# Optimization experiments

Hardware: AMD Instinct MI355X
Metric: run time of the kernel (lower is better)

Reference implementation:

```python
import jax, jax.numpy as jnp
import numpy as np

N_NODES = 20000
N_EDGES = 160000
MUL0, MUL1 = 32, 16          # 32x0e + 16x1o for both in and out irreps
EDGE_FEAT = 128
HIDDEN = 128
W_SIZES = [MUL0*MUL0, MUL1*MUL0, MUL0*MUL1, MUL1*MUL1, MUL1*MUL1]  # uvw weights per path (sh muls are 1)
W_OFF = np.cumsum([0] + W_SIZES).tolist()
W_NUMEL = W_OFF[-1]          # 2560
EPS_LN = 1e-5

_e = np.zeros((3, 3, 3), np.float32)
for i, j, k in [(0, 1, 2), (1, 2, 0), (2, 0, 1)]:
    _e[i, j, k] = 1.0
    _e[i, k, j] = -1.0
EPS3 = jnp.asarray(_e)  # Levi-Civita for 1o x 1o -> 1o path


def setup_inputs() -> dict:
    key = jax.random.key(0)
    ks = jax.random.split(key, 8)
    node_attr = jax.random.normal(ks[0], (N_NODES, MUL0 + 3 * MUL1), jnp.float32)
    edge_index = jax.random.randint(ks[1], (2, N_EDGES), 0, N_NODES)
    edge_attr = jax.random.normal(ks[2], (N_EDGES, EDGE_FEAT), jnp.float32)
    edge_sh = jax.random.normal(ks[3], (N_EDGES, 4), jnp.float32)
    s1 = float(1.0 / np.sqrt(EDGE_FEAT))
    s2 = float(1.0 / np.sqrt(HIDDEN))
    fc_w1 = jax.random.uniform(ks[4], (EDGE_FEAT, HIDDEN), jnp.float32, -s1, s1)
    fc_b1 = jnp.zeros((HIDDEN,), jnp.float32)
    fc_w2 = jax.random.uniform(ks[5], (HIDDEN, W_NUMEL), jnp.float32, -s2, s2)
    fc_b2 = jnp.zeros((W_NUMEL,), jnp.float32)
    # LayerNorm params: mean_shift is ones for scalar (0e) irreps, zeros for 1o
    mean_shift = jnp.concatenate(
        [jnp.ones((1, MUL0, 1), jnp.float32), jnp.zeros((1, MUL1, 1), jnp.float32)], axis=1)
    affine_weight = jnp.ones((MUL0 + MUL1,), jnp.float32) + 0.1 * jax.random.normal(ks[6], (MUL0 + MUL1,), jnp.float32)
    affine_bias = 0.02 * jax.random.normal(ks[7], (MUL0,), jnp.float32)
    return dict(node_attr=node_attr, edge_attr=edge_attr, edge_sh=edge_sh,
                fc_w1=fc_w1, fc_b1=fc_b1, fc_w2=fc_w2, fc_b2=fc_b2,
                mean_shift=mean_shift, affine_weight=affine_weight,
                affine_bias=affine_bias, edge_index=edge_index)


def _forward(node_attr, edge_attr, edge_sh, fc_w1, fc_b1, fc_w2, fc_b2,
             mean_shift, affine_weight, affine_bias, edge_index):
    edge_src, edge_dst = edge_index[0], edge_index[1]
    # gather source-of-message node features per edge
    x = node_attr[edge_dst]                          # [E, 80]
    x0 = x[:, :MUL0]                                 # [E, 32]   l=0 scalars
    x1 = x[:, MUL0:].reshape(-1, MUL1, 3)            # [E, 16, 3] l=1 vectors
    sh0 = edge_sh[:, 0]                              # [E]
    sh1 = edge_sh[:, 1:4]                            # [E, 3]

    # per-edge TP weights from edge features (SimpleLinear: Lin-ReLU-Lin, dropout=0)
    w = jnp.maximum(edge_attr @ fc_w1 + fc_b1, 0.0) @ fc_w2 + fc_b2   # [E, 2560]
    w1 = w[:, W_OFF[0]:W_OFF[1]].reshape(-1, MUL0, MUL0)
    w2 = w[:, W_OFF[1]:W_OFF[2]].reshape(-1, MUL1, MUL0)
    w3 = w[:, W_OFF[2]:W_OFF[3]].reshape(-1, MUL0, MUL1)
    w4 = w[:, W_OFF[3]:W_OFF[4]].reshape(-1, MUL1, MUL1)
    w5 = w[:, W_OFF[4]:W_OFF[5]].reshape(-1, MUL1, MUL1)

    # e3nn FullyConnectedTensorProduct normalization (component + element):
    # coeff = sqrt(ir_out.dim / sum_of_fan_in_over_paths_to_that_output)
    c0 = float(np.sqrt(1.0 / (MUL0 + MUL1)))            # -> 0e: fan 32+16
    c1 = float(np.sqrt(3.0 / (MUL0 + MUL1 + MUL1)))     # -> 1o: fan 32+16+16
    is3 = float(1.0 / np.sqrt(3.0))  # wigner-3j (110),(011),(101)
    is6 = float(1.0 / np.sqrt(6.0))  # wigner-3j (111)

    out0 = c0 * (jnp.einsum('eu,e,euw->ew', x0, sh0, w1)
                 + is3 * jnp.einsum('eui,ei,euw->ew', x1, sh1, w2))            # [E, 32]
    out1 = c1 * (is3 * jnp.einsum('eu,ek,euw->ewk', x0, sh1, w3)
                 + is3 * jnp.einsum('eui,e,euw->ewi', x1, sh0, w4)
                 + is6 * jnp.einsum('ijk,eui,ej,euw->ewk', EPS3, x1, sh1, w5)) # [E, 16, 3]
    tp = jnp.concatenate([out0, out1.reshape(-1, MUL1 * 3)], axis=-1)          # [E, 80]

    # scatter-mean over destination (edge_src) nodes
    seg = jax.ops.segment_sum(tp, edge_src, num_segments=N_NODES)
    cnt = jax.ops.segment_sum(jnp.ones((tp.shape[0],), tp.dtype), edge_src, num_segments=N_NODES)
    out = seg / jnp.maximum(cnt, 1.0)[:, None]

    # residual (out irreps == in irreps, so F.pad is a no-op)
    out = out + node_attr

    # equivariant LayerNorm (normalization='component')
    f0 = out[:, :MUL0].reshape(-1, MUL0, 1)
    f0 = f0 - jnp.mean(f0, axis=1, keepdims=True) * mean_shift[:, :MUL0]
    n0 = jnp.mean(jnp.mean(f0 * f0, axis=-1), axis=1, keepdims=True)           # [N, 1]
    n0 = jax.lax.rsqrt(n0 + EPS_LN) * affine_weight[None, :MUL0]               # [N, 32]
    f0 = f0 * n0[:, :, None] + affine_bias[None, :, None]

    f1 = out[:, MUL0:].reshape(-1, MUL1, 3)
    f1 = f1 - jnp.mean(f1, axis=1, keepdims=True) * mean_shift[:, MUL0:]       # mean_shift=0 here
    n1 = jnp.mean(jnp.mean(f1 * f1, axis=-1), axis=1, keepdims=True)
    n1 = jax.lax.rsqrt(n1 + EPS_LN) * affine_weight[None, MUL0:]
    f1 = f1 * n1[:, :, None]

    return jnp.concatenate([f0.reshape(-1, MUL0), f1.reshape(-1, MUL1 * 3)], axis=-1)


def reference(node_attr, edge_attr, edge_sh, fc_w1, fc_b1, fc_w2, fc_b2,
              mean_shift, affine_weight, affine_bias, edge_index):
    return _forward(node_attr, edge_attr, edge_sh, fc_w1, fc_b1, fc_w2, fc_b2,
                    mean_shift, affine_weight, affine_bias, edge_index)
```

## Files before the change

### kernel.cpp

```cpp
#include <hip/hip_runtime.h>

typedef __attribute__((ext_vector_type(8))) short short8;
typedef __attribute__((ext_vector_type(4))) short bfx4;
typedef __attribute__((ext_vector_type(4))) float floatx4;

#define N_NODES 20000
#define N_EDGES 160000
#define TILE_E 128
#define EBLK (N_EDGES / TILE_E)

#define C0f   0.14433756729740643f
#define C1f   0.21650635094610965f
#define IS3   0.5773502691896258f
#define IS6   0.4082482904638631f
#define EPS_LN 1e-5f

#define W1F_OFF 0
#define W2F_OFF 32768
#define CNT_OFF 688128

__device__ __forceinline__ short f2bf(float f) {
    unsigned u = __float_as_uint(f);
    u += 0x7fff + ((u >> 16) & 1);
    return (short)(u >> 16);
}
__device__ __forceinline__ float bf2f(short s) {
    return __uint_as_float(((unsigned)(unsigned short)s) << 16);
}

__device__ __forceinline__ short8 load8_bf16(const float* p) {
    const float4* q = (const float4*)p;
    float4 f0 = q[0], f1 = q[1];
    short8 s;
    s[0]=f2bf(f0.x); s[1]=f2bf(f0.y); s[2]=f2bf(f0.z); s[3]=f2bf(f0.w);
    s[4]=f2bf(f1.x); s[5]=f2bf(f1.y); s[6]=f2bf(f1.z); s[7]=f2bf(f1.w);
    return s;
}

__device__ __forceinline__ floatx4 mfma4(const short8* a, short8 b0, short8 b1,
                                         short8 b2, short8 b3, float bias) {
    floatx4 C = {bias, bias, bias, bias};
    C = __builtin_amdgcn_mfma_f32_16x16x32_bf16(a[0], b0, C, 0, 0, 0);
    C = __builtin_amdgcn_mfma_f32_16x16x32_bf16(a[1], b1, C, 0, 0, 0);
    C = __builtin_amdgcn_mfma_f32_16x16x32_bf16(a[2], b2, C, 0, 0, 0);
    C = __builtin_amdgcn_mfma_f32_16x16x32_bf16(a[3], b3, C, 0, 0, 0);
    return C;
}

__device__ __forceinline__ int xsw(int row, int el) {
    return row * 64 + ((el & 3) | ((((el >> 2) ^ row) & 15) << 2));
}
__device__ __forceinline__ bfx4 ldx(const short* base, int row, int gran) {
    return *(const bfx4*)(base + row * 64 + (((gran ^ row) & 15) << 2));
}

__device__ __forceinline__ int hsw(int row, int col) {
    return row * 128 + (col & 7) + ((((col >> 3) ^ (row & 15)) & 15) << 3);
}

__global__ __launch_bounds__(256)
void prep_kernel(const float* __restrict__ fc_w1, const float* __restrict__ fc_w2,
                 short* __restrict__ w1f, short* __restrict__ w2f,
                 float* __restrict__ cnt, float* __restrict__ out) {
    int g = blockIdx.x * 256 + threadIdx.x;
    if (g < N_NODES) cnt[g] = 0.0f;
    float4 z = {0.f, 0.f, 0.f, 0.f};
    for (int i = g; i < 400000; i += 43008) ((float4*)out)[i] = z;
    if (g < 2048) {
        int ln = g & 15, qd = (g >> 4) & 3, kt = (g >> 6) & 3, t = g >> 8;
        int n = t * 16 + ln, kb = kt * 32 + qd * 8;
        short8 s;
        #pragma unroll
        for (int j = 0; j < 8; ++j) s[j] = f2bf(fc_w1[(kb + j) * 128 + n]);
        *(short8*)(w1f + g * 8) = s;
    } else {
        int g2 = g - 2048;
        if (g2 < 40960) {
            int ln = g2 & 15, qd = (g2 >> 4) & 3, kt = (g2 >> 6) & 3, t = g2 >> 8;
            int n = t * 16 + ln, kb = kt * 32 + qd * 8;
            short8 s;
            #pragma unroll
            for (int j = 0; j < 8; ++j) s[j] = f2bf(fc_w2[(kb + j) * 2560 + n]);
            int p = (t < 128) ? t : (t < 144 ? 128 + 2 * (t - 128) : 129 + 2 * (t - 144));
            *(short8*)(w2f + (size_t)p * 2048 + (g2 & 255) * 8) = s;
        }
    }
}

__global__ __launch_bounds__(256, 2)
void edge_kernel(const float* __restrict__ node_attr,
                 const float* __restrict__ edge_attr,
                 const float* __restrict__ edge_sh,
                 const float* __restrict__ fc_b1,
                 const float* __restrict__ fc_b2,
                 const int*   __restrict__ edge_index,
                 const short* __restrict__ w1f,
                 const short* __restrict__ w2f,
                 float* __restrict__ accum,
                 float* __restrict__ cnt)
{
    __shared__ __align__(16) short s_pool[128 * 128];
    __shared__ __align__(16) short s_w2[2 * 4096];
    __shared__ float s_sh[128 * 4];
    __shared__ int   s_src[128];
    __shared__ int   s_dst[128];

    short* s_H    = s_pool;
    short* s_x0t  = s_pool;
    short* s_x1t  = s_pool + 4096;
    short* s_x1dt = s_pool + 10240;

    const int tid  = threadIdx.x;
    const int e0   = blockIdx.x * TILE_E;
    const int lane = tid & 63;
    const int wv   = tid >> 6;

    float4 stA, stB;
    {
        const float4* sp = (const float4*)w2f;
        stA = sp[tid]; stB = sp[tid + 256];
    }

    if (tid < 128) {
        int s = edge_index[e0 + tid];
        int d = edge_index[N_EDGES + e0 + tid];
        s_src[tid] = s; s_dst[tid] = d;
        atomicAdd(&cnt[s], 1.0f);
    }
    s_sh[tid]       = edge_sh[(size_t)e0 * 4 + tid];
    s_sh[tid + 256] = edge_sh[(size_t)e0 * 4 + tid + 256];
    __syncthreads();

    const int ln   = lane & 15;
    const int qd   = lane >> 4;
    const int eb0  = wv * 32 + qd * 4;
    const int eb1  = eb0 + 16;
    const int half = wv >> 1;
    const int gr0  = (wv & 1) * 8 + qd;
    const int gr1  = gr0 + 4;
    const short* x0b  = s_x0t  + half * 2048;
    const short* x1b  = s_x1t  + half * 3072;
    const short* x1db = s_x1dt + half * 1024;

    {
        short8 a1[2][4];
        #pragma unroll
        for (int g = 0; g < 2; ++g) {
            const float* ap = edge_attr + (size_t)(e0 + wv*32 + g*16 + ln) * 128 + qd * 8;
            #pragma unroll
            for (int kt = 0; kt < 4; ++kt) a1[g][kt] = load8_bf16(ap + kt * 32);
        }
        #pragma unroll
        for (int t = 0; t < 8; ++t) {
            const short* bp = w1f + t * 2048 + lane * 8;
            short8 b0 = *(const short8*)bp;
            short8 b1 = *(const short8*)(bp + 512);
            short8 b2 = *(const short8*)(bp + 1024);
            short8 b3 = *(const short8*)(bp + 1536);
            float bias = fc_b1[t * 16 + ln];
            #pragma unroll
            for (int g = 0; g < 2; ++g) {
                floatx4 C = mfma4(a1[g], b0, b1, b2, b3, bias);
                #pragma unroll
                for (int r = 0; r < 4; ++r)
                    s_H[hsw(wv*32 + g*16 + qd*4 + r, t*16 + ln)] = f2bf(fmaxf(C[r], 0.f));
            }
        }
    }

    short8 a2[2][4];
    #pragma unroll
    for (int g = 0; g < 2; ++g) {
        const int row = wv*32 + g*16 + ln;
        #pragma unroll
        for (int kt = 0; kt < 4; ++kt)
            a2[g][kt] = *(const short8*)(s_H + row * 128 +
                                         (((qd + 4*kt) ^ (row & 15)) << 3));
    }
    __syncthreads();

    #pragma unroll
    for (int i = 0; i < 40; ++i) {
        int f = tid + i * 256;
        int e = f / 80, c = f % 80;
        float v = node_attr[(size_t)s_dst[e] * 80 + c];
        int hf = e >> 6, el = e & 63;
        if (c < 32) s_x0t[hf * 2048 + xsw(c, el)] = f2bf(v);
        else        s_x1t[hf * 3072 + xsw(c - 32, el)] = f2bf(v);
    }
    #pragma unroll
    for (int i = 0; i < 8; ++i) {
        int it = tid + i * 256;
        int e = it >> 4, u = it & 15;
        const float* xp = node_attr + (size_t)s_dst[e] * 80 + 32 + u * 3;
        float d = xp[0] * s_sh[e*4+1] + xp[1] * s_sh[e*4+2] + xp[2] * s_sh[e*4+3];
        s_x1dt[(e >> 6) * 1024 + xsw(u, e & 63)] = f2bf(d);
    }
    {
        float4* dp = (float4*)s_w2;
        dp[tid] = stA; dp[tid + 256] = stB;
        const float4* sp = (const float4*)(w2f + 4096);
        stA = sp[tid]; stB = sp[tid + 256];
    }
    __syncthreads();

    auto stage_step = [&](int cg) {
        if (cg + 1 < 80) {
            float4* dp = (float4*)(s_w2 + ((cg + 1) & 1) * 4096);
            dp[tid] = stA; dp[tid + 256] = stB;
        }
        if (cg + 2 < 80) {
            const float4* sp = (const float4*)(w2f + (size_t)(cg + 2) * 4096);
            stA = sp[tid]; stB = sp[tid + 256];
        }
    };

    float r0lo[2][4] = {}, r0hi[2][4] = {}, r1lo[2][4] = {}, r1hi[2][4] = {};

    #pragma unroll 1
    for (int c = 0; c < 32; ++c) {
        stage_step(c);
        const short* bp = s_w2 + (c & 1) * 4096 + lane * 8;
        short8 L0 = *(const short8*)bp,          L1 = *(const short8*)(bp + 512);
        short8 L2 = *(const short8*)(bp + 1024), L3 = *(const short8*)(bp + 1536);
        short8 H0 = *(const short8*)(bp + 2048), H1 = *(const short8*)(bp + 2560);
        short8 H2 = *(const short8*)(bp + 3072), H3 = *(const short8*)(bp + 3584);
        float blo = fc_b2[c * 32 + ln], bhi = fc_b2[c * 32 + 16 + ln];
        #pragma unroll
        for (int g = 0; g < 2; ++g) {
            floatx4 Clo = mfma4(a2[g], L0, L1, L2, L3, blo);
            floatx4 Chi = mfma4(a2[g], H0, H1, H2, H3, bhi);
            bfx4 xs = ldx(x0b, c, g ? gr1 : gr0);
            #pragma unroll
            for (int r = 0; r < 4; ++r) {
                float a = bf2f(xs[r]);
                r0lo[g][r] += a * Clo[r];
                r0hi[g][r] += a * Chi[r];
            }
        }
        __syncthreads();
    }
    #pragma unroll 1
    for (int c2 = 0; c2 < 16; ++c2) {
        stage_step(32 + c2);
        const short* bp = s_w2 + ((32 + c2) & 1) * 4096 + lane * 8;
        short8 L0 = *(const short8*)bp,          L1 = *(const short8*)(bp + 512);
        short8 L2 = *(const short8*)(bp + 1024), L3 = *(const short8*)(bp + 1536);
        short8 H0 = *(const short8*)(bp + 2048), H1 = *(const short8*)(bp + 2560);
        short8 H2 = *(const short8*)(bp + 3072), H3 = *(const short8*)(bp + 3584);
        float blo = fc_b2[1024 + c2 * 32 + ln], bhi = fc_b2[1024 + c2 * 32 + 16 + ln];
        #pragma unroll
        for (int g = 0; g < 2; ++g) {
            floatx4 Clo = mfma4(a2[g], L0, L1, L2, L3, blo);
            floatx4 Chi = mfma4(a2[g], H0, H1, H2, H3, bhi);
            bfx4 xs = ldx(x1db, c2, g ? gr1 : gr0);
            #pragma unroll
            for (int r = 0; r < 4; ++r) {
                float a = bf2f(xs[r]);
                r1lo[g][r] += a * Clo[r];
                r1hi[g][r] += a * Chi[r];
            }
        }
        __syncthreads();
    }
    #pragma unroll
    for (int g = 0; g < 2; ++g)
        #pragma unroll
        for (int r = 0; r < 4; ++r) {
            int e = (g ? eb1 : eb0) + r;
            float sh0 = s_sh[e*4];
            int base = s_src[e] * 80;
            atomicAdd(&accum[base + ln],      C0f * (sh0 * r0lo[g][r] + IS3 * r1lo[g][r]));
            atomicAdd(&accum[base + 16 + ln], C0f * (sh0 * r0hi[g][r] + IS3 * r1hi[g][r]));
        }

    float r3[2][4] = {};
    float r4[2][4][3] = {};
    float r5[2][4][3] = {};

    #pragma unroll 1
    for (int c3 = 0; c3 < 16; ++c3) {
        stage_step(48 + c3);
        const short* bb = s_w2 + ((48 + c3) & 1) * 4096 + lane * 8;
        #pragma unroll
        for (int t = 0; t < 2; ++t) {
            const int u = 2 * c3 + t;
            const short* bp = bb + t * 2048;
            short8 b0 = *(const short8*)bp,          b1 = *(const short8*)(bp + 512);
            short8 b2 = *(const short8*)(bp + 1024), b3 = *(const short8*)(bp + 1536);
            float bias = fc_b2[1536 + u * 16 + ln];
            #pragma unroll
            for (int g = 0; g < 2; ++g) {
                floatx4 C = mfma4(a2[g], b0, b1, b2, b3, bias);
                bfx4 xs = ldx(x0b, u, g ? gr1 : gr0);
                #pragma unroll
                for (int r = 0; r < 4; ++r)
                    r3[g][r] += bf2f(xs[r]) * C[r];
            }
        }
        __syncthreads();
    }
    #pragma unroll 1
    for (int c4 = 0; c4 < 16; ++c4) {
        const int cg = 64 + c4;
        stage_step(cg);
        const short* bb = s_w2 + (cg & 1) * 4096 + lane * 8;
        short8 F0 = *(const short8*)bb,          F1 = *(const short8*)(bb + 512);
        short8 F2 = *(const short8*)(bb + 1024), F3 = *(const short8*)(bb + 1536);
        short8 G0 = *(const short8*)(bb + 2048), G1 = *(const short8*)(bb + 2560);
        short8 G2 = *(const short8*)(bb + 3072), G3 = *(const short8*)(bb + 3584);
        float b4 = fc_b2[2048 + c4 * 16 + ln], b5 = fc_b2[2304 + c4 * 16 + ln];
        #pragma unroll
        for (int g = 0; g < 2; ++g) {
            floatx4 C4 = mfma4(a2[g], F0, F1, F2, F3, b4);
            floatx4 C5 = mfma4(a2[g], G0, G1, G2, G3, b5);
            int gr = (g ? gr1 : gr0);
            bfx4 x0s = ldx(x1b, c4*3 + 0, gr);
            bfx4 x1s = ldx(x1b, c4*3 + 1, gr);
            bfx4 x2s = ldx(x1b, c4*3 + 2, gr);
            #pragma unroll
            for (int r = 0; r < 4; ++r) {
                float a0 = bf2f(x0s[r]), a1 = bf2f(x1s[r]), a2v = bf2f(x2s[r]);
                r4[g][r][0] += a0 * C4[r];  r5[g][r][0] += a0 * C5[r];
                r4[g][r][1] += a1 * C4[r];  r5[g][r][1] += a1 * C5[r];
                r4[g][r][2] += a2v * C4[r]; r5[g][r][2] += a2v * C5[r];
            }
        }
        if (c4 < 15) __syncthreads();
    }
    #pragma unroll
    for (int g = 0; g < 2; ++g)
        #pragma unroll
        for (int r = 0; r < 4; ++r) {
            int e = (g ? eb1 : eb0) + r;
            float sh0 = s_sh[e*4], sa = s_sh[e*4+1], sb = s_sh[e*4+2], sc = s_sh[e*4+3];
            int base = s_src[e] * 80;
            float t3 = C1f * IS3 * r3[g][r];
            float s0 = C1f * IS3 * sh0;
            float c6 = C1f * IS6;
            float v50 = r5[g][r][1] * sc - r5[g][r][2] * sb;
            float v51 = r5[g][r][2] * sa - r5[g][r][0] * sc;
            float v52 = r5[g][r][0] * sb - r5[g][r][1] * sa;
            atomicAdd(&accum[base + 32 + ln*3 + 0], sa * t3 + s0 * r4[g][r][0] + c6 * v50);
            atomicAdd(&accum[base + 32 + ln*3 + 1], sb * t3 + s0 * r4[g][r][1] + c6 * v51);
            atomicAdd(&accum[base + 32 + ln*3 + 2], sc * t3 + s0 * r4[g][r][2] + c6 * v52);
        }
}

__global__ __launch_bounds__(256)
void node_kernel(const float* __restrict__ node_attr,
                 const float* __restrict__ mean_shift,
                 const float* __restrict__ aw,
                 const float* __restrict__ ab,
                 const float* __restrict__ cnt,
                 float* __restrict__ out)
{
    __shared__ float sv[64 * 85];
    __shared__ float s_inv[64];
    const int tid = threadIdx.x;
    const int n0  = blockIdx.x * 64;

    if (tid < 64) {
        int n = n0 + tid;
        s_inv[tid] = (n < N_NODES) ? 1.0f / fmaxf(cnt[n], 1.0f) : 0.0f;
    }
    __syncthreads();

    #pragma unroll
    for (int i = 0; i < 20; ++i) {
        int idx = tid + i * 256;
        int r = idx / 80, cch = idx % 80;
        int n = n0 + r;
        if (n < N_NODES) {
            float o = out[(size_t)n * 80 + cch];
            float a = node_attr[(size_t)n * 80 + cch];
            sv[r * 85 + cch] = o * s_inv[r] + a;
        }
    }
    __syncthreads();

    if (tid < 64 && n0 + tid < N_NODES) {
        float v[80];
        const float* sp = sv + tid * 85;
        #pragma unroll
        for (int k = 0; k < 80; ++k) v[k] = sp[k];

        float m0 = 0.f;
        #pragma unroll
        for (int u = 0; u < 32; ++u) m0 += v[u];
        m0 *= (1.0f / 32.0f);
        float n0v = 0.f;
        #pragma unroll
        for (int u = 0; u < 32; ++u) {
            float f = v[u] - m0 * mean_shift[u];
            v[u] = f;
            n0v += f * f;
        }
        n0v = rsqrtf(n0v * (1.0f / 32.0f) + EPS_LN);
        #pragma unroll
        for (int u = 0; u < 32; ++u) v[u] = v[u] * (n0v * aw[u]) + ab[u];

        float m1[3] = {0.f, 0.f, 0.f};
        #pragma unroll
        for (int u = 0; u < 16; ++u)
            #pragma unroll
            for (int i = 0; i < 3; ++i) m1[i] += v[32 + u*3 + i];
        #pragma unroll
        for (int i = 0; i < 3; ++i) m1[i] *= (1.0f / 16.0f);
        float n1 = 0.f;
        #pragma unroll
        for (int u = 0; u < 16; ++u)
            #pragma unroll
            for (int i = 0; i < 3; ++i) {
                float f = v[32 + u*3 + i] - m1[i] * mean_shift[32 + u];
                v[32 + u*3 + i] = f;
                n1 += f * f;
            }
        n1 = rsqrtf(n1 * (1.0f / 48.0f) + EPS_LN);
        #pragma unroll
        for (int u = 0; u < 16; ++u)
            #pragma unroll
            for (int i = 0; i < 3; ++i)
                v[32 + u*3 + i] *= (n1 * aw[32 + u]);

        float* wp = sv + tid * 85;
        #pragma unroll
        for (int k = 0; k < 80; ++k) wp[k] = v[k];
    }
    __syncthreads();

    #pragma unroll
    for (int i = 0; i < 20; ++i) {
        int idx = tid + i * 256;
        int r = idx / 80, cch = idx % 80;
        int n = n0 + r;
        if (n < N_NODES) out[(size_t)n * 80 + cch] = sv[r * 85 + cch];
    }
}

extern "C" void kernel_launch(void* const* d_in, const int* in_sizes, int n_in,
                              void* d_out, int out_size, void* d_ws, size_t ws_size,
                              hipStream_t stream) {
    const float* node_attr  = (const float*)d_in[0];
    const float* edge_attr  = (const float*)d_in[1];
    const float* edge_sh    = (const float*)d_in[2];
    const float* fc_w1      = (const float*)d_in[3];
    const float* fc_b1      = (const float*)d_in[4];
    const float* fc_w2      = (const float*)d_in[5];
    const float* fc_b2      = (const float*)d_in[6];
    const float* mean_shift = (const float*)d_in[7];
    const float* aw         = (const float*)d_in[8];
    const float* ab         = (const float*)d_in[9];
    const int*   edge_index = (const int*)d_in[10];
    float* out = (float*)d_out;

    short* w1f = (short*)((char*)d_ws + W1F_OFF);
    short* w2f = (short*)((char*)d_ws + W2F_OFF);
    float* cnt = (float*)((char*)d_ws + CNT_OFF);

    prep_kernel<<<(2048 + 40960 + 255) / 256, 256, 0, stream>>>(fc_w1, fc_w2, w1f, w2f,
                                                                cnt, out);
    edge_kernel<<<EBLK, 256, 0, stream>>>(node_attr, edge_attr, edge_sh,
                                          fc_b1, fc_b2, edge_index,
                                          w1f, w2f, out, cnt);
    node_kernel<<<(N_NODES + 63) / 64, 256, 0, stream>>>(node_attr, mean_shift,
                                                         aw, ab, cnt, out);
}
```

Before: 363.3 us.

## Use two waves per edge tile, each handling 64 edges

The edge kernel now runs 128 threads (2 waves) per 128-edge tile instead of 4 waves, so each wave processes 64 edges (4 row groups) rather than 32. Each B fragment of the weight matrix loaded from LDS is reused across four MFMAs instead of two, which halves LDS reads of weights per edge. Per-thread staging of weights grows to four float4 registers. The cost is fewer waves per CU to hide latency and much higher register pressure, since the accumulator arrays double and could spill under launch_bounds(128,2).

```diff
diff --git a/kernel.cpp b/kernel.cpp
--- a/kernel.cpp
+++ b/kernel.cpp
@@ -87,7 +87,7 @@
     }
 }
 
-__global__ __launch_bounds__(256, 2)
+__global__ __launch_bounds__(128, 2)
 void edge_kernel(const float* __restrict__ node_attr,
                  const float* __restrict__ edge_attr,
                  const float* __restrict__ edge_sh,
@@ -115,38 +115,35 @@
     const int lane = tid & 63;
     const int wv   = tid >> 6;
 
-    float4 stA, stB;
+    float4 stA, stB, stC, stD;
     {
         const float4* sp = (const float4*)w2f;
-        stA = sp[tid]; stB = sp[tid + 256];
-    }
-
-    if (tid < 128) {
+        stA = sp[tid]; stB = sp[tid + 128]; stC = sp[tid + 256]; stD = sp[tid + 384];
+    }
+
+    {
         int s = edge_index[e0 + tid];
         int d = edge_index[N_EDGES + e0 + tid];
         s_src[tid] = s; s_dst[tid] = d;
         atomicAdd(&cnt[s], 1.0f);
     }
-    s_sh[tid]       = edge_sh[(size_t)e0 * 4 + tid];
-    s_sh[tid + 256] = edge_sh[(size_t)e0 * 4 + tid + 256];
+    #pragma unroll
+    for (int i = 0; i < 4; ++i)
+        s_sh[tid + i * 128] = edge_sh[(size_t)e0 * 4 + tid + i * 128];
     __syncthreads();
 
     const int ln   = lane & 15;
     const int qd   = lane >> 4;
-    const int eb0  = wv * 32 + qd * 4;
-    const int eb1  = eb0 + 16;
-    const int half = wv >> 1;
-    const int gr0  = (wv & 1) * 8 + qd;
-    const int gr1  = gr0 + 4;
-    const short* x0b  = s_x0t  + half * 2048;
-    const short* x1b  = s_x1t  + half * 3072;
-    const short* x1db = s_x1dt + half * 1024;
+    const int grn[4] = {qd, 4 + qd, 8 + qd, 12 + qd};
+    const short* x0b  = s_x0t  + wv * 2048;
+    const short* x1b  = s_x1t  + wv * 3072;
+    const short* x1db = s_x1dt + wv * 1024;
 
     {
-        short8 a1[2][4];
-        #pragma unroll
-        for (int g = 0; g < 2; ++g) {
-            const float* ap = edge_attr + (size_t)(e0 + wv*32 + g*16 + ln) * 128 + qd * 8;
+        short8 a1[4][4];
+        #pragma unroll
+        for (int g = 0; g < 4; ++g) {
+            const float* ap = edge_attr + (size_t)(e0 + wv*64 + g*16 + ln) * 128 + qd * 8;
             #pragma unroll
             for (int kt = 0; kt < 4; ++kt) a1[g][kt] = load8_bf16(ap + kt * 32);
         }
@@ -159,19 +156,19 @@
             short8 b3 = *(const short8*)(bp + 1536);
             float bias = fc_b1[t * 16 + ln];
             #pragma unroll
-            for (int g = 0; g < 2; ++g) {
+            for (int g = 0; g < 4; ++g) {
                 floatx4 C = mfma4(a1[g], b0, b1, b2, b3, bias);
                 #pragma unroll
                 for (int r = 0; r < 4; ++r)
-                    s_H[hsw(wv*32 + g*16 + qd*4 + r, t*16 + ln)] = f2bf(fmaxf(C[r], 0.f));
-            }
-        }
-    }
-
-    short8 a2[2][4];
-    #pragma unroll
-    for (int g = 0; g < 2; ++g) {
-        const int row = wv*32 + g*16 + ln;
+                    s_H[hsw(wv*64 + g*16 + qd*4 + r, t*16 + ln)] = f2bf(fmaxf(C[r], 0.f));
+            }
+        }
+    }
+
+    short8 a2[4][4];
+    #pragma unroll
+    for (int g = 0; g < 4; ++g) {
+        const int row = wv*64 + g*16 + ln;
         #pragma unroll
         for (int kt = 0; kt < 4; ++kt)
             a2[g][kt] = *(const short8*)(s_H + row * 128 +
@@ -179,9 +176,9 @@
     }
     __syncthreads();
 
-    #pragma unroll
-    for (int i = 0; i < 40; ++i) {
-        int f = tid + i * 256;
+    #pragma unroll 8
+    for (int i = 0; i < 80; ++i) {
+        int f = tid + i * 128;
         int e = f / 80, c = f % 80;
         float v = node_attr[(size_t)s_dst[e] * 80 + c];
         int hf = e >> 6, el = e & 63;
@@ -189,8 +186,8 @@
         else        s_x1t[hf * 3072 + xsw(c - 32, el)] = f2bf(v);
     }
     #pragma unroll
-    for (int i = 0; i < 8; ++i) {
-        int it = tid + i * 256;
+    for (int i = 0; i < 16; ++i) {
+        int it = tid + i * 128;
         int e = it >> 4, u = it & 15;
         const float* xp = node_attr + (size_t)s_dst[e] * 80 + 32 + u * 3;
         float d = xp[0] * s_sh[e*4+1] + xp[1] * s_sh[e*4+2] + xp[2] * s_sh[e*4+3];
@@ -198,24 +195,24 @@
     }
     {
         float4* dp = (float4*)s_w2;
-        dp[tid] = stA; dp[tid + 256] = stB;
+        dp[tid] = stA; dp[tid+128] = stB; dp[tid+256] = stC; dp[tid+384] = stD;
         const float4* sp = (const float4*)(w2f + 4096);
-        stA = sp[tid]; stB = sp[tid + 256];
+        stA = sp[tid]; stB = sp[tid+128]; stC = sp[tid+256]; stD = sp[tid+384];
     }
     __syncthreads();
 
     auto stage_step = [&](int cg) {
         if (cg + 1 < 80) {
             float4* dp = (float4*)(s_w2 + ((cg + 1) & 1) * 4096);
-            dp[tid] = stA; dp[tid + 256] = stB;
+            dp[tid] = stA; dp[tid+128] = stB; dp[tid+256] = stC; dp[tid+384] = stD;
         }
         if (cg + 2 < 80) {
             const float4* sp = (const float4*)(w2f + (size_t)(cg + 2) * 4096);
-            stA = sp[tid]; stB = sp[tid + 256];
+            stA = sp[tid]; stB = sp[tid+128]; stC = sp[tid+256]; stD = sp[tid+384];
         }
     };
 
-    float r0lo[2][4] = {}, r0hi[2][4] = {}, r1lo[2][4] = {}, r1hi[2][4] = {};
+    float r0lo[4][4] = {}, r0hi[4][4] = {}, r1lo[4][4] = {}, r1hi[4][4] = {};
 
     #pragma unroll 1
     for (int c = 0; c < 32; ++c) {
@@ -227,10 +224,10 @@
         short8 H2 = *(const short8*)(bp + 3072), H3 = *(const short8*)(bp + 3584);
         float blo = fc_b2[c * 32 + ln], bhi = fc_b2[c * 32 + 16 + ln];
         #pragma unroll
-        for (int g = 0; g < 2; ++g) {
+        for (int g = 0; g < 4; ++g) {
             floatx4 Clo = mfma4(a2[g], L0, L1, L2, L3, blo);
             floatx4 Chi = mfma4(a2[g], H0, H1, H2, H3, bhi);
-            bfx4 xs = ldx(x0b, c, g ? gr1 : gr0);
+            bfx4 xs = ldx(x0b, c, grn[g]);
             #pragma unroll
             for (int r = 0; r < 4; ++r) {
                 float a = bf2f(xs[r]);
@@ -250,10 +247,10 @@
         short8 H2 = *(const short8*)(bp + 3072), H3 = *(const short8*)(bp + 3584);
         float blo = fc_b2[1024 + c2 * 32 + ln], bhi = fc_b2[1024 + c2 * 32 + 16 + ln];
         #pragma unroll
-        for (int g = 0; g < 2; ++g) {
+        for (int g = 0; g < 4; ++g) {
             floatx4 Clo = mfma4(a2[g], L0, L1, L2, L3, blo);
             floatx4 Chi = mfma4(a2[g], H0, H1, H2, H3, bhi);
-            bfx4 xs = ldx(x1db, c2, g ? gr1 : gr0);
+            bfx4 xs = ldx(x1db, c2, grn[g]);
             #pragma unroll
             for (int r = 0; r < 4; ++r) {
                 float a = bf2f(xs[r]);
@@ -264,19 +261,19 @@
         __syncthreads();
     }
     #pragma unroll
-    for (int g = 0; g < 2; ++g)
+    for (int g = 0; g < 4; ++g)
         #pragma unroll
         for (int r = 0; r < 4; ++r) {
-            int e = (g ? eb1 : eb0) + r;
+            int e = wv*64 + g*16 + qd*4 + r;
             float sh0 = s_sh[e*4];
             int base = s_src[e] * 80;
             atomicAdd(&accum[base + ln],      C0f * (sh0 * r0lo[g][r] + IS3 * r1lo[g][r]));
             atomicAdd(&accum[base + 16 + ln], C0f * (sh0 * r0hi[g][r] + IS3 * r1hi[g][r]));
         }
 
-    float r3[2][4] = {};
-    float r4[2][4][3] = {};
-    float r5[2][4][3] = {};
+    float r3[4][4] = {};
+    float r4[4][4][3] = {};
+    float r5[4][4][3] = {};
 
     #pragma unroll 1
     for (int c3 = 0; c3 < 16; ++c3) {
@@ -290,9 +287,9 @@
             short8 b2 = *(const short8*)(bp + 1024), b3 = *(const short8*)(bp + 1536);
             float bias = fc_b2[1536 + u * 16 + ln];
             #pragma unroll
-            for (int g = 0; g < 2; ++g) {
+            for (int g = 0; g < 4; ++g) {
                 floatx4 C = mfma4(a2[g], b0, b1, b2, b3, bias);
-                bfx4 xs = ldx(x0b, u, g ? gr1 : gr0);
+                bfx4 xs = ldx(x0b, u, grn[g]);
                 #pragma unroll
                 for (int r = 0; r < 4; ++r)
                     r3[g][r] += bf2f(xs[r]) * C[r];
@@ -311,13 +308,12 @@
         short8 G2 = *(const short8*)(bb + 3072), G3 = *(const short8*)(bb + 3584);
         float b4 = fc_b2[2048 + c4 * 16 + ln], b5 = fc_b2[2304 + c4 * 16 + ln];
         #pragma unroll
-        for (int g = 0; g < 2; ++g) {
+        for (int g = 0; g < 4; ++g) {
             floatx4 C4 = mfma4(a2[g], F0, F1, F2, F3, b4);
             floatx4 C5 = mfma4(a2[g], G0, G1, G2, G3, b5);
-            int gr = (g ? gr1 : gr0);
-            bfx4 x0s = ldx(x1b, c4*3 + 0, gr);
-            bfx4 x1s = ldx(x1b, c4*3 + 1, gr);
-            bfx4 x2s = ldx(x1b, c4*3 + 2, gr);
+            bfx4 x0s = ldx(x1b, c4*3 + 0, grn[g]);
+            bfx4 x1s = ldx(x1b, c4*3 + 1, grn[g]);
+            bfx4 x2s = ldx(x1b, c4*3 + 2, grn[g]);
             #pragma unroll
             for (int r = 0; r < 4; ++r) {
                 float a0 = bf2f(x0s[r]), a1 = bf2f(x1s[r]), a2v = bf2f(x2s[r]);
@@ -329,10 +325,10 @@
         if (c4 < 15) __syncthreads();
     }
     #pragma unroll
-    for (int g = 0; g < 2; ++g)
+    for (int g = 0; g < 4; ++g)
         #pragma unroll
         for (int r = 0; r < 4; ++r) {
-            int e = (g ? eb1 : eb0) + r;
+            int e = wv*64 + g*16 + qd*4 + r;
             float sh0 = s_sh[e*4], sa = s_sh[e*4+1], sb = s_sh[e*4+2], sc = s_sh[e*4+3];
             int base = s_src[e] * 80;
             float t3 = C1f * IS3 * r3[g][r];
@@ -460,7 +456,7 @@
 
     prep_kernel<<<(2048 + 40960 + 255) / 256, 256, 0, stream>>>(fc_w1, fc_w2, w1f, w2f,
                                                                 cnt, out);
-    edge_kernel<<<EBLK, 256, 0, stream>>>(node_attr, edge_attr, edge_sh,
+    edge_kernel<<<EBLK, 128, 0, stream>>>(node_attr, edge_attr, edge_sh,
                                           fc_b1, fc_b2, edge_index,
                                           w1f, w2f, out, cnt);
     node_kernel<<<(N_NODES + 63) / 64, 256, 0, stream>>>(node_attr, mean_shift,
```

Result: slower. 434.3 us (+19.5%).
